# Optimization experiments

Measured on AMD Instinct MI355X. Metric: run time of the kernel, lower is better.

Reference implementation:

```python
import jax, jax.numpy as jnp
import numpy as np

RANGES = {"measure": 256, "beat": 16, "position": 128, "duration": 128, "pitch": 256,
          "instrument": 129, "velocity": 128, "key_sign": 24, "time_sign": 48, "tempo": 49}
R_TOTAL = sum(RANGES.values())  # 1162
NUMERATORS = jnp.array([1, 2, 3, 4, 5, 6, 7, 8, 9, 10, 12, 16], dtype=jnp.int32)
TOT_NUM = 12
NEG = jnp.float32(-1e9)


def _prefix_gather(x, axis=1):
    # value at position i becomes the cumulative value at index min(i+1, S-1):
    # reproduces the tf mask `range(S) <= idx+1` (prefix up to i+1 inclusive).
    S = x.shape[axis]
    idx = jnp.minimum(jnp.arange(S) + 1, S - 1)
    return jnp.take(x, idx, axis=axis)


def _present_mask(song, dtype_id, feat, R):
    # occ[b,i,v] = True iff some token j<=i+1 has type dtype_id and song[b,j,feat]==v
    # (vectorized form of tensor_scatter_nd_max over a prefix, via one-hot + cummax)
    match = song[..., 0] == dtype_id                       # [B,S]
    onehot = (song[..., feat][..., None] == jnp.arange(R)) & match[..., None]
    cum = jax.lax.cummax(onehot.astype(jnp.int32), axis=1)
    return _prefix_gather(cum, 1).astype(bool)             # [B,S,R]


def _has_any(song, dtype_id):
    match = (song[..., 0] == dtype_id).astype(jnp.int32)
    return _prefix_gather(jax.lax.cummax(match, axis=1), 1).astype(bool)  # [B,S]


def _last_value(song, dtype_id, feat):
    # song[b, argmax_j(match*j) , feat] over the prefix j<=i+1; tf argmax of all
    # zeros returns 0, reproduced by where(match, j, 0) + cummax.
    match = song[..., 0] == dtype_id
    j = jnp.arange(song.shape[1])
    last_idx = _prefix_gather(jax.lax.cummax(jnp.where(match, j, 0), axis=1), 1)
    return jnp.take_along_axis(song[..., feat], last_idx, axis=1)  # [B,S]


def _forward(song, chosen_type, scores):
    B, S, _ = song.shape
    Rm, Rb = RANGES["measure"], RANGES["beat"]
    ar_m = jnp.arange(RANGES["measure"]); ar_b = jnp.arange(RANGES["beat"])
    ar_p = jnp.arange(RANGES["position"])
    ar_ks = jnp.arange(RANGES["key_sign"]); ar_ts = jnp.arange(RANGES["time_sign"])
    ar_tp = jnp.arange(RANGES["tempo"])
    t = chosen_type[..., None]  # [B,S,1]

    inst_present = _present_mask(song, 1, 6, RANGES["instrument"])  # [B,S,129]
    has_inst = inst_present.any(-1, keepdims=True)

    last_ks = _last_value(song, 4, 8);  oh_ks = last_ks[..., None] == ar_ks
    last_ts = _last_value(song, 5, 9);  oh_ts = last_ts[..., None] == ar_ts
    last_tp = _last_value(song, 6, 10); oh_tp = last_tp[..., None] == ar_tp
    has_ks = _has_any(song, 4)[..., None]
    has_ts = _has_any(song, 5)[..., None]

    # ---- chosen_type == 3 (note-like token) ----
    min_measure = song[..., 1]
    pred_m = jnp.argmax(scores[..., :Rm], axis=-1).astype(jnp.int32)
    c1 = pred_m == min_measure
    min_beat = jnp.where(c1, song[..., 2], 0)
    pred_b = jnp.argmax(scores[..., Rm:Rm + Rb], axis=-1).astype(jnp.int32)
    c2 = c1 & (pred_b == min_beat)
    min_pos = jnp.where(c2, song[..., 3], 0)
    max_beat = NUMERATORS[jnp.mod(last_ts, TOT_NUM)]  # get_max_beat_from_time_sign
    m3 = ar_m >= min_measure[..., None]
    b3 = (ar_b >= min_beat[..., None]) & (ar_b < max_beat[..., None])
    p3 = ar_p >= min_pos[..., None]

    # ---- chosen_type == 1 (instrument): forbid already-present instruments ----
    inst1 = jnp.where(has_inst, ~inst_present, True)

    # ---- chosen_type in 4..6 (key_sign / time_sign / tempo) ----
    min_m46 = jnp.where((song[..., 2] == 0) & (song[..., 3] == 0),
                        song[..., 1], song[..., 1] + 1)
    m46 = ar_m >= min_m46[..., None]
    ks4 = jnp.where(has_ks, ~oh_ks, True)
    ts5 = jnp.where(has_ts, ~oh_ts, True)
    tp6 = ~oh_tp

    is3 = t == 3
    measure_mask = jnp.where(is3, m3, jnp.where((t >= 4) & (t <= 6), m46, True))
    beat_mask = jnp.where(is3, b3, True)
    position_mask = jnp.where(is3, p3, True)
    duration_mask = jnp.ones((B, S, RANGES["duration"]), bool)
    pitch_mask = jnp.ones((B, S, RANGES["pitch"]), bool)
    instrument_mask = jnp.where(is3, inst_present, jnp.where(t == 1, inst1, True))
    velocity_mask = jnp.ones((B, S, RANGES["velocity"]), bool)
    key_sign_mask = jnp.where(is3, oh_ks, jnp.where(t == 4, ks4, True))
    time_sign_mask = jnp.where(is3, oh_ts, jnp.where(t == 5, ts5, True))
    tempo_mask = jnp.where(is3, oh_tp, jnp.where(t == 6, tp6, True))

    mask = jnp.concatenate([measure_mask, beat_mask, position_mask, duration_mask,
                            pitch_mask, instrument_mask, velocity_mask,
                            key_sign_mask, time_sign_mask, tempo_mask], axis=-1)
    return jnp.where(mask, scores, NEG)  # masked logits [B,S,R_TOTAL]


def setup_inputs() -> dict:
    key = jax.random.key(0)
    k_song, k_type, k_scores = jax.random.split(key, 3)
    B, S = 8, 2047  # SEQ_LEN-1 with SEQ_LEN=2048
    col_max = [8, RANGES["measure"], RANGES["beat"], RANGES["position"],
               RANGES["duration"], RANGES["pitch"], RANGES["instrument"],
               RANGES["velocity"], RANGES["key_sign"], RANGES["time_sign"],
               RANGES["tempo"]]
    kcols = jax.random.split(k_song, 11)
    song = jnp.stack([jax.random.randint(kcols[c], (B, S), 0, col_max[c],
                                         dtype=jnp.int32) for c in range(11)], axis=-1)
    chosen_type = jax.random.randint(k_type, (B, S), 0, 8, dtype=jnp.int32)
    scores = jax.random.normal(k_scores, (B, S, R_TOTAL), dtype=jnp.float32)
    return {"song": song, "chosen_type": chosen_type, "scores": scores}


def reference(song, chosen_type, scores):
    return _forward(song, chosen_type, scores)
```

## Files before the change

kernel.cpp:

```cpp
#include <hip/hip_runtime.h>
#include <cstdint>
#include <cstddef>

#define S_LEN 2047
#define BATCH 8
#define R_TOT 1162
#define NEGV (-1e9f)

__device__ __constant__ int d_numerators[12] = {1, 2, 3, 4, 5, 6, 7, 8, 9, 10, 12, 16};

__global__ __launch_bounds__(256) void scan_kernel(const int* __restrict__ song,
                                                   unsigned* __restrict__ state) {
    const int b = blockIdx.x;
    const int tid = threadIdx.x;
    __shared__ unsigned lds_f[3][256];
    __shared__ unsigned lds_inst[5][256];
    __shared__ unsigned bc[8];
    const unsigned HAS = 1u << 16;
    const long base = (long)b * S_LEN;

    unsigned c_f[3];
    unsigned c_inst[5] = {0, 0, 0, 0, 0};
    {
        const int* r0 = song + base * 11;
        c_f[0] = (unsigned)r0[8];
        c_f[1] = (unsigned)r0[9];
        c_f[2] = (unsigned)r0[10];
    }

    for (int chunk = 0; chunk < S_LEN; chunk += 256) {
        const int j = chunk + tid;
        unsigned e_f[3] = {0, 0, 0};
        unsigned e_inst[5] = {0, 0, 0, 0, 0};
        if (j < S_LEN) {
            const int* rj = song + (base + j) * 11;
            const int type = rj[0];
            if (type == 4)      e_f[0] = HAS | (unsigned)rj[8];
            else if (type == 5) e_f[1] = HAS | (unsigned)rj[9];
            else if (type == 6) e_f[2] = HAS | (unsigned)rj[10];
            else if (type == 1) { const int v = rj[6]; e_inst[v >> 5] = 1u << (v & 31); }
        }
#pragma unroll
        for (int w = 0; w < 3; w++) lds_f[w][tid] = e_f[w];
#pragma unroll
        for (int w = 0; w < 5; w++) lds_inst[w][tid] = e_inst[w];
        __syncthreads();

        for (int off = 1; off < 256; off <<= 1) {
            unsigned p_f[3] = {0, 0, 0};
            unsigned p_inst[5] = {0, 0, 0, 0, 0};
            if (tid >= off) {
#pragma unroll
                for (int w = 0; w < 3; w++) p_f[w] = lds_f[w][tid - off];
#pragma unroll
                for (int w = 0; w < 5; w++) p_inst[w] = lds_inst[w][tid - off];
            }
            __syncthreads();
            if (tid >= off) {
#pragma unroll
                for (int w = 0; w < 3; w++) {
                    if (!(e_f[w] & HAS)) e_f[w] = p_f[w];
                    lds_f[w][tid] = e_f[w];
                }
#pragma unroll
                for (int w = 0; w < 5; w++) {
                    e_inst[w] |= p_inst[w];
                    lds_inst[w][tid] = e_inst[w];
                }
            }
            __syncthreads();
        }

        unsigned t_f[3], t_inst[5];
#pragma unroll
        for (int w = 0; w < 3; w++) t_f[w] = (e_f[w] & HAS) ? e_f[w] : c_f[w];
#pragma unroll
        for (int w = 0; w < 5; w++) t_inst[w] = e_inst[w] | c_inst[w];

        if (j < S_LEN) {
            const unsigned pack =
                (t_f[0] & 0xFFu) | ((t_f[1] & 0xFFu) << 8) | ((t_f[2] & 0xFFu) << 16) |
                (((t_f[0] >> 16) & 1u) << 24) | (((t_f[1] >> 16) & 1u) << 25);
            unsigned* sp = state + (size_t)(base + j) * 6;
            sp[0] = pack;
#pragma unroll
            for (int w = 0; w < 5; w++) sp[1 + w] = t_inst[w];
        }

        const int last = min(255, S_LEN - 1 - chunk);
        if (tid == last) {
#pragma unroll
            for (int w = 0; w < 3; w++) bc[w] = t_f[w];
#pragma unroll
            for (int w = 0; w < 5; w++) bc[3 + w] = t_inst[w];
        }
        __syncthreads();
#pragma unroll
        for (int w = 0; w < 3; w++) c_f[w] = bc[w];
#pragma unroll
        for (int w = 0; w < 5; w++) c_inst[w] = bc[3 + w];
        __syncthreads();
    }
}

__global__ __launch_bounds__(256) void mask_kernel(const int* __restrict__ song,
                                                   const int* __restrict__ ctype,
                                                   const float* __restrict__ scores,
                                                   const unsigned* __restrict__ state,
                                                   float* __restrict__ out) {
    const int row = blockIdx.x;
    const int tid = threadIdx.x;
    const int b = row / S_LEN;
    const int i = row - b * S_LEN;

    __shared__ float s_val[128];
    __shared__ int   s_idx[128];
    __shared__ float sb_val[8];
    __shared__ int   sb_idx[8];
    __shared__ int   s_info[10];
    __shared__ int   f_info[17];

    const size_t rbase = (size_t)row * R_TOT;
    const float2* s2 = (const float2*)(scores + rbase);
    float2* o2 = (float2*)(out + rbase);

    const float2 r0 = s2[tid];
    const float2 r1 = s2[tid + 256];
    float2 r2 = make_float2(0.f, 0.f);
    if (tid < 69) r2 = s2[tid + 512];

    if (tid < 128) {
        const bool sec = (r0.y > r0.x);
        s_val[tid] = sec ? r0.y : r0.x;
        s_idx[tid] = 2 * tid + (sec ? 1 : 0);
    } else if (tid < 136) {
        const bool sec = (r0.y > r0.x);
        sb_val[tid - 128] = sec ? r0.y : r0.x;
        sb_idx[tid - 128] = (2 * tid - 256) + (sec ? 1 : 0);
    } else if (tid < 142) {
        const int e = min(i + 1, S_LEN - 1);
        s_info[tid - 136] = (int)state[((size_t)b * S_LEN + e) * 6 + (tid - 136)];
    } else if (tid < 146) {
        const int* srow = song + (size_t)row * 11;
        if (tid == 142) s_info[6] = srow[1];
        if (tid == 143) s_info[7] = srow[2];
        if (tid == 144) s_info[8] = srow[3];
        if (tid == 145) s_info[9] = ctype[row];
    }
    __syncthreads();

    for (int s = 64; s > 0; s >>= 1) {
        if (tid < s) {
            if (s_val[tid + s] > s_val[tid]) {
                s_val[tid] = s_val[tid + s];
                s_idx[tid] = s_idx[tid + s];
            }
        }
        __syncthreads();
    }

    if (tid == 0) {
        const int pred_m = s_idx[0];
        float bv = sb_val[0];
        int pred_b = sb_idx[0];
#pragma unroll
        for (int q = 1; q < 8; q++) {
            if (sb_val[q] > bv) { bv = sb_val[q]; pred_b = sb_idx[q]; }
        }
        const unsigned pack = (unsigned)s_info[0];
        const int song1 = s_info[6], song2 = s_info[7], song3 = s_info[8];
        const int t = s_info[9];
        const bool c1 = (pred_m == song1);
        const int min_beat = c1 ? song2 : 0;
        const bool c2 = c1 && (pred_b == min_beat);
        const int min_pos = c2 ? song3 : 0;
        const int last_ks = pack & 0xFF;
        const int last_ts = (pack >> 8) & 0xFF;
        const int last_tp = (pack >> 16) & 0xFF;
        f_info[0] = t;
        f_info[1] = song1;
        f_info[2] = min_beat;
        f_info[3] = min_pos;
        f_info[4] = (song2 == 0 && song3 == 0) ? song1 : song1 + 1;
        f_info[5] = d_numerators[last_ts % 12];
        f_info[6] = last_ks;
        f_info[7] = last_ts;
        f_info[8] = last_tp;
        f_info[9]  = (int)((pack >> 24) & 1u);
        f_info[10] = (int)((pack >> 25) & 1u);
        const unsigned u = (unsigned)s_info[1] | (unsigned)s_info[2] | (unsigned)s_info[3] |
                           (unsigned)s_info[4] | (unsigned)s_info[5];
        f_info[11] = (u != 0u);
        f_info[12] = s_info[1]; f_info[13] = s_info[2]; f_info[14] = s_info[3];
        f_info[15] = s_info[4]; f_info[16] = s_info[5];
    }
    __syncthreads();

    const int t = f_info[0];
    const int min_measure = f_info[1], min_beat = f_info[2], min_pos = f_info[3];
    const int min_m46 = f_info[4], max_beat = f_info[5];
    const int last_ks = f_info[6], last_ts = f_info[7], last_tp = f_info[8];
    const bool has_ks = f_info[9] != 0, has_ts = f_info[10] != 0, has_inst = f_info[11] != 0;
    unsigned inst[5];
#pragma unroll
    for (int w = 0; w < 5; w++) inst[w] = (unsigned)f_info[12 + w];
    const bool is3 = (t == 3);
    const bool is46 = (t >= 4) && (t <= 6);

    auto maskf = [&](int col) -> bool {
        if (col < 256) {
            if (is3) return col >= min_measure;
            if (is46) return col >= min_m46;
            return true;
        } else if (col < 272) {
            if (!is3) return true;
            const int v = col - 256;
            return (v >= min_beat) && (v < max_beat);
        } else if (col < 400) {
            return is3 ? ((col - 272) >= min_pos) : true;
        } else if (col < 784) {
            return true;
        } else if (col < 913) {
            const int v = col - 784;
            const bool pres = ((inst[v >> 5] >> (v & 31)) & 1u) != 0u;
            if (is3) return pres;
            if (t == 1) return has_inst ? !pres : true;
            return true;
        } else if (col < 1041) {
            return true;
        } else if (col < 1065) {
            const int v = col - 1041;
            if (is3) return v == last_ks;
            if (t == 4) return has_ks ? (v != last_ks) : true;
            return true;
        } else if (col < 1113) {
            const int v = col - 1065;
            if (is3) return v == last_ts;
            if (t == 5) return has_ts ? (v != last_ts) : true;
            return true;
        } else {
            const int v = col - 1113;
            if (is3) return v == last_tp;
            if (t == 6) return v != last_tp;
            return true;
        }
    };

    float2 w;
    int c = 2 * tid;
    w.x = maskf(c)     ? r0.x : NEGV;
    w.y = maskf(c + 1) ? r0.y : NEGV;
    o2[tid] = w;

    c = 512 + 2 * tid;
    w.x = maskf(c)     ? r1.x : NEGV;
    w.y = maskf(c + 1) ? r1.y : NEGV;
    o2[tid + 256] = w;

    if (tid < 69) {
        c = 1024 + 2 * tid;
        w.x = maskf(c)     ? r2.x : NEGV;
        w.y = maskf(c + 1) ? r2.y : NEGV;
        o2[tid + 512] = w;
    }
}

extern "C" void kernel_launch(void* const* d_in, const int* in_sizes, int n_in,
                              void* d_out, int out_size, void* d_ws, size_t ws_size,
                              hipStream_t stream) {
    const int* song = (const int*)d_in[0];
    const int* ctype = (const int*)d_in[1];
    const float* scores = (const float*)d_in[2];
    float* out = (float*)d_out;
    unsigned* state = (unsigned*)d_ws;

    scan_kernel<<<BATCH, 256, 0, stream>>>(song, state);
    mask_kernel<<<BATCH * S_LEN, 256, 0, stream>>>(song, ctype, scores, state, out);
}
```

Measured before the change: 171.2 us.

## Split mask kernel into per-row parameter kernel and streaming apply kernel

Splits the fused mask kernel in two. The first kernel computes each row's argmax-dependent mask parameters from the first 512 scores and writes them to a workspace buffer. The second kernel streams the scores and applies the mask using those parameters, with no shared-memory reduction or block barrier. This is meant to shorten the dependency chain in the bandwidth-bound apply pass. The cost is an extra launch, a second read of the first part of each row, and a small round trip of the parameters through global memory.

```diff
diff --git a/kernel.cpp b/kernel.cpp
--- a/kernel.cpp
+++ b/kernel.cpp
@@ -6,6 +6,9 @@
 #define BATCH 8
 #define R_TOT 1162
 #define NEGV (-1e9f)
+
+#define PARAM_OFF 393024
+#define PSTRIDE 20
 
 __device__ __constant__ int d_numerators[12] = {1, 2, 3, 4, 5, 6, 7, 8, 9, 10, 12, 16};
 
@@ -103,11 +106,11 @@
     }
 }
 
-__global__ __launch_bounds__(256) void mask_kernel(const int* __restrict__ song,
-                                                   const int* __restrict__ ctype,
-                                                   const float* __restrict__ scores,
-                                                   const unsigned* __restrict__ state,
-                                                   float* __restrict__ out) {
+__global__ __launch_bounds__(256) void param_kernel(const int* __restrict__ song,
+                                                    const int* __restrict__ ctype,
+                                                    const float* __restrict__ scores,
+                                                    const unsigned* __restrict__ state,
+                                                    int* __restrict__ params) {
     const int row = blockIdx.x;
     const int tid = threadIdx.x;
     const int b = row / S_LEN;
@@ -118,16 +121,11 @@
     __shared__ float sb_val[8];
     __shared__ int   sb_idx[8];
     __shared__ int   s_info[10];
-    __shared__ int   f_info[17];
 
     const size_t rbase = (size_t)row * R_TOT;
     const float2* s2 = (const float2*)(scores + rbase);
-    float2* o2 = (float2*)(out + rbase);
 
     const float2 r0 = s2[tid];
-    const float2 r1 = s2[tid + 256];
-    float2 r2 = make_float2(0.f, 0.f);
-    if (tid < 69) r2 = s2[tid + 512];
 
     if (tid < 128) {
         const bool sec = (r0.y > r0.x);
@@ -174,36 +172,53 @@
         const int min_beat = c1 ? song2 : 0;
         const bool c2 = c1 && (pred_b == min_beat);
         const int min_pos = c2 ? song3 : 0;
-        const int last_ks = pack & 0xFF;
-        const int last_ts = (pack >> 8) & 0xFF;
-        const int last_tp = (pack >> 16) & 0xFF;
-        f_info[0] = t;
-        f_info[1] = song1;
-        f_info[2] = min_beat;
-        f_info[3] = min_pos;
-        f_info[4] = (song2 == 0 && song3 == 0) ? song1 : song1 + 1;
-        f_info[5] = d_numerators[last_ts % 12];
-        f_info[6] = last_ks;
-        f_info[7] = last_ts;
-        f_info[8] = last_tp;
-        f_info[9]  = (int)((pack >> 24) & 1u);
-        f_info[10] = (int)((pack >> 25) & 1u);
+        const int last_ks = (int)(pack & 0xFFu);
+        const int last_ts = (int)((pack >> 8) & 0xFFu);
+        const int last_tp = (int)((pack >> 16) & 0xFFu);
         const unsigned u = (unsigned)s_info[1] | (unsigned)s_info[2] | (unsigned)s_info[3] |
                            (unsigned)s_info[4] | (unsigned)s_info[5];
-        f_info[11] = (u != 0u);
-        f_info[12] = s_info[1]; f_info[13] = s_info[2]; f_info[14] = s_info[3];
-        f_info[15] = s_info[4]; f_info[16] = s_info[5];
-    }
-    __syncthreads();
-
-    const int t = f_info[0];
-    const int min_measure = f_info[1], min_beat = f_info[2], min_pos = f_info[3];
-    const int min_m46 = f_info[4], max_beat = f_info[5];
-    const int last_ks = f_info[6], last_ts = f_info[7], last_tp = f_info[8];
-    const bool has_ks = f_info[9] != 0, has_ts = f_info[10] != 0, has_inst = f_info[11] != 0;
+        int* pp = params + (size_t)row * PSTRIDE;
+        pp[0] = t;
+        pp[1] = song1;
+        pp[2] = min_beat;
+        pp[3] = min_pos;
+        pp[4] = (song2 == 0 && song3 == 0) ? song1 : song1 + 1;
+        pp[5] = d_numerators[last_ts % 12];
+        pp[6] = last_ks;
+        pp[7] = last_ts;
+        pp[8] = last_tp;
+        pp[9]  = (int)((pack >> 24) & 1u);
+        pp[10] = (int)((pack >> 25) & 1u);
+        pp[11] = (u != 0u);
+        pp[12] = s_info[1]; pp[13] = s_info[2]; pp[14] = s_info[3];
+        pp[15] = s_info[4]; pp[16] = s_info[5];
+    }
+}
+
+__global__ __launch_bounds__(256) void apply_kernel(const float* __restrict__ scores,
+                                                    const int* __restrict__ params,
+                                                    float* __restrict__ out) {
+    const int row = blockIdx.x;
+    const int tid = threadIdx.x;
+
+    const size_t rbase = (size_t)row * R_TOT;
+    const float2* s2 = (const float2*)(scores + rbase);
+    float2* o2 = (float2*)(out + rbase);
+
+    const float2 r0 = s2[tid];
+    const float2 r1 = s2[tid + 256];
+    float2 r2 = make_float2(0.f, 0.f);
+    if (tid < 69) r2 = s2[tid + 512];
+
+    const int* pp = params + (size_t)row * PSTRIDE;
+    const int t = pp[0];
+    const int min_measure = pp[1], min_beat = pp[2], min_pos = pp[3];
+    const int min_m46 = pp[4], max_beat = pp[5];
+    const int last_ks = pp[6], last_ts = pp[7], last_tp = pp[8];
+    const bool has_ks = pp[9] != 0, has_ts = pp[10] != 0, has_inst = pp[11] != 0;
     unsigned inst[5];
 #pragma unroll
-    for (int w = 0; w < 5; w++) inst[w] = (unsigned)f_info[12 + w];
+    for (int w = 0; w < 5; w++) inst[w] = (unsigned)pp[12 + w];
     const bool is3 = (t == 3);
     const bool is46 = (t >= 4) && (t <= 6);
 
@@ -273,7 +288,9 @@
     const float* scores = (const float*)d_in[2];
     float* out = (float*)d_out;
     unsigned* state = (unsigned*)d_ws;
+    int* params = (int*)((char*)d_ws + PARAM_OFF);
 
     scan_kernel<<<BATCH, 256, 0, stream>>>(song, state);
-    mask_kernel<<<BATCH * S_LEN, 256, 0, stream>>>(song, ctype, scores, state, out);
-}
+    param_kernel<<<BATCH * S_LEN, 256, 0, stream>>>(song, ctype, scores, state, params);
+    apply_kernel<<<BATCH * S_LEN, 256, 0, stream>>>(scores, params, out);
+}
```

After: 181.2 us. 5.9% more time.

## Split sequential per-batch scan into parallel chunk scans plus carry pass

Applied to the files above, without the earlier changes.

Replaces the single-block-per-batch sequential chunk scan with 64 independent chunk-local scans, a tiny carry-propagation kernel, and combines local prefix and chunk carry inside the mask kernel. This removes the serial chain of eight chunk scans per batch that ran on only eight blocks. It adds an extra kernel launch and a second state read per row in the mask kernel.

```diff
diff --git a/kernel.cpp b/kernel.cpp
--- a/kernel.cpp
+++ b/kernel.cpp
@@ -5,108 +5,108 @@
 #define S_LEN 2047
 #define BATCH 8
 #define R_TOT 1162
+#define NCHUNK 8
 #define NEGV (-1e9f)
 
+#define CARRY_OFF 393024
+
 __device__ __constant__ int d_numerators[12] = {1, 2, 3, 4, 5, 6, 7, 8, 9, 10, 12, 16};
 
-__global__ __launch_bounds__(256) void scan_kernel(const int* __restrict__ song,
-                                                   unsigned* __restrict__ state) {
-    const int b = blockIdx.x;
+__global__ __launch_bounds__(256) void scan_local(const int* __restrict__ song,
+                                                  unsigned* __restrict__ local) {
+    const int b = blockIdx.x >> 3;
+    const int c = blockIdx.x & 7;
     const int tid = threadIdx.x;
+    const int j = c * 256 + tid;
     __shared__ unsigned lds_f[3][256];
     __shared__ unsigned lds_inst[5][256];
-    __shared__ unsigned bc[8];
     const unsigned HAS = 1u << 16;
     const long base = (long)b * S_LEN;
 
-    unsigned c_f[3];
-    unsigned c_inst[5] = {0, 0, 0, 0, 0};
-    {
-        const int* r0 = song + base * 11;
-        c_f[0] = (unsigned)r0[8];
-        c_f[1] = (unsigned)r0[9];
-        c_f[2] = (unsigned)r0[10];
-    }
-
-    for (int chunk = 0; chunk < S_LEN; chunk += 256) {
-        const int j = chunk + tid;
-        unsigned e_f[3] = {0, 0, 0};
-        unsigned e_inst[5] = {0, 0, 0, 0, 0};
-        if (j < S_LEN) {
-            const int* rj = song + (base + j) * 11;
-            const int type = rj[0];
-            if (type == 4)      e_f[0] = HAS | (unsigned)rj[8];
-            else if (type == 5) e_f[1] = HAS | (unsigned)rj[9];
-            else if (type == 6) e_f[2] = HAS | (unsigned)rj[10];
-            else if (type == 1) { const int v = rj[6]; e_inst[v >> 5] = 1u << (v & 31); }
-        }
-#pragma unroll
-        for (int w = 0; w < 3; w++) lds_f[w][tid] = e_f[w];
-#pragma unroll
-        for (int w = 0; w < 5; w++) lds_inst[w][tid] = e_inst[w];
+    unsigned e_f[3] = {0, 0, 0};
+    unsigned e_inst[5] = {0, 0, 0, 0, 0};
+    if (j < S_LEN) {
+        const int* rj = song + (base + j) * 11;
+        const int type = rj[0];
+        if (type == 4)      e_f[0] = HAS | (unsigned)rj[8];
+        else if (type == 5) e_f[1] = HAS | (unsigned)rj[9];
+        else if (type == 6) e_f[2] = HAS | (unsigned)rj[10];
+        else if (type == 1) { const int v = rj[6]; e_inst[v >> 5] = 1u << (v & 31); }
+    }
+#pragma unroll
+    for (int w = 0; w < 3; w++) lds_f[w][tid] = e_f[w];
+#pragma unroll
+    for (int w = 0; w < 5; w++) lds_inst[w][tid] = e_inst[w];
+    __syncthreads();
+
+    for (int off = 1; off < 256; off <<= 1) {
+        unsigned p_f[3] = {0, 0, 0};
+        unsigned p_inst[5] = {0, 0, 0, 0, 0};
+        if (tid >= off) {
+#pragma unroll
+            for (int w = 0; w < 3; w++) p_f[w] = lds_f[w][tid - off];
+#pragma unroll
+            for (int w = 0; w < 5; w++) p_inst[w] = lds_inst[w][tid - off];
+        }
         __syncthreads();
-
-        for (int off = 1; off < 256; off <<= 1) {
-            unsigned p_f[3] = {0, 0, 0};
-            unsigned p_inst[5] = {0, 0, 0, 0, 0};
-            if (tid >= off) {
-#pragma unroll
-                for (int w = 0; w < 3; w++) p_f[w] = lds_f[w][tid - off];
-#pragma unroll
-                for (int w = 0; w < 5; w++) p_inst[w] = lds_inst[w][tid - off];
+        if (tid >= off) {
+#pragma unroll
+            for (int w = 0; w < 3; w++) {
+                if (!(e_f[w] & HAS)) e_f[w] = p_f[w];
+                lds_f[w][tid] = e_f[w];
             }
-            __syncthreads();
-            if (tid >= off) {
-#pragma unroll
-                for (int w = 0; w < 3; w++) {
-                    if (!(e_f[w] & HAS)) e_f[w] = p_f[w];
-                    lds_f[w][tid] = e_f[w];
-                }
-#pragma unroll
-                for (int w = 0; w < 5; w++) {
-                    e_inst[w] |= p_inst[w];
-                    lds_inst[w][tid] = e_inst[w];
-                }
+#pragma unroll
+            for (int w = 0; w < 5; w++) {
+                e_inst[w] |= p_inst[w];
+                lds_inst[w][tid] = e_inst[w];
             }
-            __syncthreads();
-        }
-
-        unsigned t_f[3], t_inst[5];
-#pragma unroll
-        for (int w = 0; w < 3; w++) t_f[w] = (e_f[w] & HAS) ? e_f[w] : c_f[w];
-#pragma unroll
-        for (int w = 0; w < 5; w++) t_inst[w] = e_inst[w] | c_inst[w];
-
-        if (j < S_LEN) {
-            const unsigned pack =
-                (t_f[0] & 0xFFu) | ((t_f[1] & 0xFFu) << 8) | ((t_f[2] & 0xFFu) << 16) |
-                (((t_f[0] >> 16) & 1u) << 24) | (((t_f[1] >> 16) & 1u) << 25);
-            unsigned* sp = state + (size_t)(base + j) * 6;
-            sp[0] = pack;
-#pragma unroll
-            for (int w = 0; w < 5; w++) sp[1 + w] = t_inst[w];
-        }
-
-        const int last = min(255, S_LEN - 1 - chunk);
-        if (tid == last) {
-#pragma unroll
-            for (int w = 0; w < 3; w++) bc[w] = t_f[w];
-#pragma unroll
-            for (int w = 0; w < 5; w++) bc[3 + w] = t_inst[w];
         }
         __syncthreads();
-#pragma unroll
-        for (int w = 0; w < 3; w++) c_f[w] = bc[w];
-#pragma unroll
-        for (int w = 0; w < 5; w++) c_inst[w] = bc[3 + w];
-        __syncthreads();
+    }
+
+    if (j < S_LEN) {
+        const unsigned w0 =
+            (e_f[0] & 0xFFu) | ((e_f[1] & 0xFFu) << 8) | ((e_f[2] & 0xFFu) << 16) |
+            (((e_f[0] >> 16) & 1u) << 24) | (((e_f[1] >> 16) & 1u) << 25) |
+            (((e_f[2] >> 16) & 1u) << 26);
+        unsigned* sp = local + (size_t)(base + j) * 6;
+        sp[0] = w0;
+#pragma unroll
+        for (int w = 0; w < 5; w++) sp[1 + w] = e_inst[w];
+    }
+}
+
+__global__ __launch_bounds__(64) void scan_carry(const int* __restrict__ song,
+                                                 const unsigned* __restrict__ local,
+                                                 unsigned* __restrict__ carry) {
+    const int b = threadIdx.x;
+    if (b >= BATCH) return;
+    const int* r0 = song + (size_t)b * S_LEN * 11;
+    unsigned cks = (unsigned)r0[8], cts = (unsigned)r0[9], ctp = (unsigned)r0[10];
+    unsigned chas = 0;
+    unsigned cinst[5] = {0, 0, 0, 0, 0};
+    for (int c = 0; c < NCHUNK; c++) {
+        unsigned* cp = carry + ((size_t)b * NCHUNK + c) * 6;
+        cp[0] = (cks & 0xFFu) | ((cts & 0xFFu) << 8) | ((ctp & 0xFFu) << 16) | (chas << 24);
+#pragma unroll
+        for (int w = 0; w < 5; w++) cp[1 + w] = cinst[w];
+        const int pos = min((c + 1) * 256, S_LEN) - 1;
+        const unsigned* lp = local + ((size_t)b * S_LEN + pos) * 6;
+        const unsigned a0 = lp[0];
+        if ((a0 >> 24) & 1u) cks = a0 & 0xFFu;
+        if ((a0 >> 25) & 1u) cts = (a0 >> 8) & 0xFFu;
+        if ((a0 >> 26) & 1u) ctp = (a0 >> 16) & 0xFFu;
+        chas |= (a0 >> 24) & 7u;
+#pragma unroll
+        for (int w = 0; w < 5; w++) cinst[w] |= lp[1 + w];
     }
 }
 
 __global__ __launch_bounds__(256) void mask_kernel(const int* __restrict__ song,
                                                    const int* __restrict__ ctype,
                                                    const float* __restrict__ scores,
-                                                   const unsigned* __restrict__ state,
+                                                   const unsigned* __restrict__ local,
+                                                   const unsigned* __restrict__ carry,
                                                    float* __restrict__ out) {
     const int row = blockIdx.x;
     const int tid = threadIdx.x;
@@ -138,8 +138,22 @@
         sb_val[tid - 128] = sec ? r0.y : r0.x;
         sb_idx[tid - 128] = (2 * tid - 256) + (sec ? 1 : 0);
     } else if (tid < 142) {
+        const int w = tid - 136;
         const int e = min(i + 1, S_LEN - 1);
-        s_info[tid - 136] = (int)state[((size_t)b * S_LEN + e) * 6 + (tid - 136)];
+        const unsigned lw = local[((size_t)b * S_LEN + e) * 6 + w];
+        const unsigned cw = carry[((size_t)b * NCHUNK + (e >> 8)) * 6 + w];
+        unsigned v;
+        if (w == 0) {
+            const unsigned ks = ((lw >> 24) & 1u) ? (lw & 0xFFu) : (cw & 0xFFu);
+            const unsigned ts = ((lw >> 25) & 1u) ? ((lw >> 8) & 0xFFu) : ((cw >> 8) & 0xFFu);
+            const unsigned tp = ((lw >> 26) & 1u) ? ((lw >> 16) & 0xFFu) : ((cw >> 16) & 0xFFu);
+            const unsigned hks = ((lw >> 24) | (cw >> 24)) & 1u;
+            const unsigned hts = ((lw >> 25) | (cw >> 25)) & 1u;
+            v = ks | (ts << 8) | (tp << 16) | (hks << 24) | (hts << 25);
+        } else {
+            v = lw | cw;
+        }
+        s_info[w] = (int)v;
     } else if (tid < 146) {
         const int* srow = song + (size_t)row * 11;
         if (tid == 142) s_info[6] = srow[1];
@@ -272,8 +286,10 @@
     const int* ctype = (const int*)d_in[1];
     const float* scores = (const float*)d_in[2];
     float* out = (float*)d_out;
-    unsigned* state = (unsigned*)d_ws;
-
-    scan_kernel<<<BATCH, 256, 0, stream>>>(song, state);
-    mask_kernel<<<BATCH * S_LEN, 256, 0, stream>>>(song, ctype, scores, state, out);
-}
+    unsigned* local = (unsigned*)d_ws;
+    unsigned* carry = (unsigned*)((char*)d_ws + CARRY_OFF);
+
+    scan_local<<<BATCH * NCHUNK, 256, 0, stream>>>(song, local);
+    scan_carry<<<1, 64, 0, stream>>>(song, local, carry);
+    mask_kernel<<<BATCH * S_LEN, 256, 0, stream>>>(song, ctype, scores, local, carry, out);
+}
```

After: 154.2 us. -9.9%, faster.
